# Performance work log

Measured on AMD Instinct MI355X. Metric: run time of the kernel, lower is better.

Reference implementation:

```python
import jax, jax.numpy as jnp
import numpy as np

N_NODES = 20000
N_EDGES = 320000
N_QUERY = 100000
D = 256


def _sage_conv(x, adj_row, adj_col, Wl, bl, Wr):
    # PyG SAGEConv with mean aggregation over SparseTensor adj_t:
    #   out = lin_l(mean_{j in N(i)} x_j) + lin_r(x_i)
    # adj_row = destination node, adj_col = source node.
    n = x.shape[0]
    msg = x[adj_col]                                        # [E, D] gather
    agg = jax.ops.segment_sum(msg, adj_row, num_segments=n)  # [N, D]
    deg = jax.ops.segment_sum(jnp.ones((adj_row.shape[0],), x.dtype), adj_row,
                              num_segments=n)
    agg = agg / jnp.maximum(deg, 1.0)[:, None]               # mean reduce
    return agg @ Wl + bl + x @ Wr


def setup_inputs() -> dict:
    key = jax.random.key(0)
    ks = jax.random.split(key, 12)
    s = 1.0 / np.sqrt(D)
    return {
        "adj_row": jax.random.randint(ks[0], (N_EDGES,), 0, N_NODES, dtype=jnp.int32),
        "adj_col": jax.random.randint(ks[1], (N_EDGES,), 0, N_NODES, dtype=jnp.int32),
        "edges": jax.random.randint(ks[2], (2, N_QUERY), 0, N_NODES, dtype=jnp.int32),
        "emb": jax.random.normal(ks[3], (N_NODES, D), jnp.float32),
        "W1l": jax.random.normal(ks[4], (D, D), jnp.float32) * s,
        "b1": jnp.zeros((D,), jnp.float32),
        "W1r": jax.random.normal(ks[5], (D, D), jnp.float32) * s,
        "W2l": jax.random.normal(ks[6], (D, D), jnp.float32) * s,
        "b2": jnp.zeros((D,), jnp.float32),
        "W2r": jax.random.normal(ks[7], (D, D), jnp.float32) * s,
        "Wp1": jax.random.normal(ks[8], (D, D), jnp.float32) * s,
        "bp1": jnp.zeros((D,), jnp.float32),
        "Wp2": jax.random.normal(ks[9], (D, 1), jnp.float32) * s,
        "bp2": jnp.zeros((1,), jnp.float32),
    }


def reference(adj_row, adj_col, edges, emb, W1l, b1, W1r, W2l, b2, W2r,
              Wp1, bp1, Wp2, bp2):
    # SAGE backbone (eval mode: dropout is identity)
    x = _sage_conv(emb, adj_row, adj_col, W1l, b1, W1r)
    x = jax.nn.relu(x)
    x = _sage_conv(x, adj_row, adj_col, W2l, b2, W2r)     # [N, D]
    # LinkPredictor: h = x_i * x_j -> MLP -> sigmoid
    h = x[edges[0]] * x[edges[1]]                          # [Q, D]
    h = jax.nn.relu(h @ Wp1 + bp1)
    return jax.nn.sigmoid(h @ Wp2 + bp2)                   # [Q, 1]
```

## Files before the change

### kernel.cpp

```cpp
#include <hip/hip_runtime.h>
#include <cstddef>

constexpr int NN = 20000;
constexpr int NE = 320000;
constexpr int NQ = 100000;
constexpr int DD = 256;
constexpr int NB = (NN + 255) / 256;
constexpr int CASTB = (NN * DD / 8 + 255) / 256;

typedef __attribute__((ext_vector_type(8))) short bf16x8;
typedef __attribute__((ext_vector_type(4))) float f32x4;
typedef __attribute__((ext_vector_type(4))) unsigned short u16x4;
typedef __attribute__((ext_vector_type(8))) unsigned short u16x8;

__device__ inline unsigned short f2bf(float f) {
    union { float f; unsigned u; } v; v.f = f;
    unsigned r = v.u + 0x7fffu + ((v.u >> 16) & 1u);
    return (unsigned short)(r >> 16);
}
__device__ inline float bf2f(unsigned short h) {
    union { unsigned u; float f; } t; t.u = ((unsigned)h) << 16;
    return t.f;
}

__global__ __launch_bounds__(256) void k_castpack(
    const float* __restrict__ x, unsigned short* __restrict__ y,
    int* __restrict__ deg,
    const float* __restrict__ w0, const float* __restrict__ w1,
    const float* __restrict__ w2, const float* __restrict__ w3,
    const float* __restrict__ w4,
    unsigned short* __restrict__ h0, unsigned short* __restrict__ h1,
    unsigned short* __restrict__ h2, unsigned short* __restrict__ h3,
    unsigned short* __restrict__ h4,
    unsigned short* __restrict__ l0, unsigned short* __restrict__ l1,
    unsigned short* __restrict__ l2, unsigned short* __restrict__ l3) {
    const int bid = blockIdx.x;
    if (bid < CASTB) {
        int i = bid * 256 + threadIdx.x;
        if (i < NN) deg[i] = 0;
        if (i >= NN * DD / 8) return;
        float4 f0 = *reinterpret_cast<const float4*>(x + (size_t)i * 8);
        float4 f1 = *reinterpret_cast<const float4*>(x + (size_t)i * 8 + 4);
        u16x8 o;
        o[0] = f2bf(f0.x); o[1] = f2bf(f0.y); o[2] = f2bf(f0.z); o[3] = f2bf(f0.w);
        o[4] = f2bf(f1.x); o[5] = f2bf(f1.y); o[6] = f2bf(f1.z); o[7] = f2bf(f1.w);
        *reinterpret_cast<u16x8*>(y + (size_t)i * 8) = o;
        return;
    }
    int mb = bid - CASTB;
    int m = mb >> 5;
    int idx = (mb & 31) * 256 + threadIdx.x;
    const float* W = (m == 0) ? w0 : (m == 1) ? w1 : (m == 2) ? w2 : (m == 3) ? w3 : w4;
    unsigned short* H = (m == 0) ? h0 : (m == 1) ? h1 : (m == 2) ? h2 : (m == 3) ? h3 : h4;
    unsigned short* L = (m == 0) ? l0 : (m == 1) ? l1 : (m == 2) ? l2 : (m == 3) ? l3 : nullptr;
    int t = idx >> 6, lane = idx & 63;
    int kt = t >> 4, nt = t & 15;
    int k0 = kt * 32 + (lane >> 4) * 8;
    int n = nt * 16 + (lane & 15);
    unsigned uh[4], ul[4];
#pragma unroll
    for (int i = 0; i < 4; ++i) {
        float fa = W[(size_t)(k0 + 2 * i) * DD + n];
        float fb = W[(size_t)(k0 + 2 * i + 1) * DD + n];
        unsigned short ha = f2bf(fa), hb = f2bf(fb);
        unsigned short la = f2bf(fa - bf2f(ha)), lb = f2bf(fb - bf2f(hb));
        uh[i] = (unsigned)ha | ((unsigned)hb << 16);
        ul[i] = (unsigned)la | ((unsigned)lb << 16);
    }
    *reinterpret_cast<uint4*>(H + (size_t)idx * 8) = make_uint4(uh[0], uh[1], uh[2], uh[3]);
    if (L)
        *reinterpret_cast<uint4*>(L + (size_t)idx * 8) = make_uint4(ul[0], ul[1], ul[2], ul[3]);
}

__global__ __launch_bounds__(256) void k_deg(const int* __restrict__ row,
                                             int* __restrict__ deg) {
    int e = blockIdx.x * 256 + threadIdx.x;
    if (e < NE) atomicAdd(&deg[row[e]], 1);
}

__global__ __launch_bounds__(256) void k_scan1(const int* __restrict__ deg,
                                               int* __restrict__ offs,
                                               int* __restrict__ bsum) {
    __shared__ int wsum[4];
    const int tid = threadIdx.x, lane = tid & 63, wid = tid >> 6;
    int i = blockIdx.x * 256 + tid;
    int v = (i < NN) ? deg[i] : 0;
    int sc = v;
#pragma unroll
    for (int d = 1; d < 64; d <<= 1) {
        int t = __shfl_up(sc, d);
        if (lane >= d) sc += t;
    }
    if (lane == 63) wsum[wid] = sc;
    __syncthreads();
    int wpre = 0;
    for (int w = 0; w < wid; ++w) wpre += wsum[w];
    if (i < NN) offs[i] = wpre + sc - v;
    if (tid == 255) bsum[blockIdx.x] = wpre + sc;
}

__global__ __launch_bounds__(256) void k_scan2(int* __restrict__ bsum) {
    __shared__ int wsum[4];
    const int tid = threadIdx.x, lane = tid & 63, wid = tid >> 6;
    int v = (tid < NB) ? bsum[tid] : 0;
    int sc = v;
#pragma unroll
    for (int d = 1; d < 64; d <<= 1) {
        int t = __shfl_up(sc, d);
        if (lane >= d) sc += t;
    }
    if (lane == 63) wsum[wid] = sc;
    __syncthreads();
    int wpre = 0;
    for (int w = 0; w < wid; ++w) wpre += wsum[w];
    if (tid < NB) bsum[tid] = wpre + sc - v;
}

__global__ __launch_bounds__(256) void k_scan3(const int* __restrict__ deg,
                                               const int* __restrict__ bsum,
                                               int* __restrict__ offs,
                                               int* __restrict__ cursor,
                                               float* __restrict__ recip) {
    int i = blockIdx.x * 256 + threadIdx.x;
    if (i < NN) {
        int o = offs[i] + bsum[i >> 8];
        offs[i] = o;
        cursor[i] = o;
        recip[i] = 1.0f / fmaxf((float)deg[i], 1.0f);
    }
    if (i == 0) offs[NN] = NE;
}

__global__ __launch_bounds__(256) void k_fill(const int* __restrict__ row,
                                              const int* __restrict__ col,
                                              int* __restrict__ cursor,
                                              int* __restrict__ scol) {
    int e = blockIdx.x * 256 + threadIdx.x;
    if (e < NE) {
        int r = row[e];
        int p = atomicAdd(&cursor[r], 1);
        scol[p] = col[e];
    }
}

__global__ __launch_bounds__(256) void k_lin(
    const unsigned short* __restrict__ A,
    const unsigned short* __restrict__ Wlh, const unsigned short* __restrict__ Wll,
    const unsigned short* __restrict__ Wrh, const unsigned short* __restrict__ Wrl,
    unsigned short* __restrict__ P, unsigned short* __restrict__ Q) {
    const int ns   = blockIdx.x & 7;
    const int mblk = blockIdx.x >> 3;
    const int wave = threadIdx.x >> 6;
    const int lane = threadIdx.x & 63;
    const int row0 = mblk * 128 + wave * 32;
    const int kcol = (lane >> 4) * 8;
    const int ar0 = min(row0 + (lane & 15), NN - 1);
    const int ar1 = min(row0 + 16 + (lane & 15), NN - 1);

    f32x4 accP[2][2], accQ[2][2];
#pragma unroll
    for (int mt = 0; mt < 2; ++mt)
#pragma unroll
        for (int nt = 0; nt < 2; ++nt) {
            accP[mt][nt] = {0, 0, 0, 0};
            accQ[mt][nt] = {0, 0, 0, 0};
        }

#pragma unroll 2
    for (int kt = 0; kt < 8; ++kt) {
        bf16x8 a0 = *reinterpret_cast<const bf16x8*>(A + (size_t)ar0 * DD + kt * 32 + kcol);
        bf16x8 a1 = *reinterpret_cast<const bf16x8*>(A + (size_t)ar1 * DD + kt * 32 + kcol);
#pragma unroll
        for (int nt = 0; nt < 2; ++nt) {
            const size_t fo = ((size_t)((kt * 16 + ns * 2 + nt) * 64 + lane)) * 8;
            bf16x8 blh = *reinterpret_cast<const bf16x8*>(Wlh + fo);
            bf16x8 bll = *reinterpret_cast<const bf16x8*>(Wll + fo);
            bf16x8 brh = *reinterpret_cast<const bf16x8*>(Wrh + fo);
            bf16x8 brl = *reinterpret_cast<const bf16x8*>(Wrl + fo);
            accP[0][nt] = __builtin_amdgcn_mfma_f32_16x16x32_bf16(a0, blh, accP[0][nt], 0, 0, 0);
            accP[1][nt] = __builtin_amdgcn_mfma_f32_16x16x32_bf16(a1, blh, accP[1][nt], 0, 0, 0);
            accP[0][nt] = __builtin_amdgcn_mfma_f32_16x16x32_bf16(a0, bll, accP[0][nt], 0, 0, 0);
            accP[1][nt] = __builtin_amdgcn_mfma_f32_16x16x32_bf16(a1, bll, accP[1][nt], 0, 0, 0);
            accQ[0][nt] = __builtin_amdgcn_mfma_f32_16x16x32_bf16(a0, brh, accQ[0][nt], 0, 0, 0);
            accQ[1][nt] = __builtin_amdgcn_mfma_f32_16x16x32_bf16(a1, brh, accQ[1][nt], 0, 0, 0);
            accQ[0][nt] = __builtin_amdgcn_mfma_f32_16x16x32_bf16(a0, brl, accQ[0][nt], 0, 0, 0);
            accQ[1][nt] = __builtin_amdgcn_mfma_f32_16x16x32_bf16(a1, brl, accQ[1][nt], 0, 0, 0);
        }
    }

    const int n0 = lane & 15;
    const int rg = (lane >> 4) * 4;
#pragma unroll
    for (int mt = 0; mt < 2; ++mt)
#pragma unroll
        for (int nt = 0; nt < 2; ++nt) {
            int n = (ns * 2 + nt) * 16 + n0;
#pragma unroll
            for (int j = 0; j < 4; ++j) {
                int r = row0 + mt * 16 + rg + j;
                if (r < NN) {
                    P[(size_t)r * DD + n] = f2bf(accP[mt][nt][j]);
                    Q[(size_t)r * DD + n] = f2bf(accQ[mt][nt][j]);
                }
            }
        }
}

template <int RELU>
__global__ __launch_bounds__(256) void k_gath(const int* __restrict__ offs,
                                              const int* __restrict__ scol,
                                              const float* __restrict__ recip,
                                              const unsigned short* __restrict__ P,
                                              const unsigned short* __restrict__ Q,
                                              const float* __restrict__ b,
                                              unsigned short* __restrict__ out) {
    int node = blockIdx.x * 4 + (threadIdx.x >> 6);
    int lane = threadIdx.x & 63;
    if (node >= NN) return;
    int s = offs[node];
    int e = offs[node + 1];
    const int half = lane >> 5;
    const int l32 = lane & 31;
    float a0[8] = {0,0,0,0,0,0,0,0}, a1[8] = {0,0,0,0,0,0,0,0};
    float a2[8] = {0,0,0,0,0,0,0,0}, a3[8] = {0,0,0,0,0,0,0,0};
    int p = s;
    for (; p + 7 < e; p += 8) {
        int base = p + 4 * half;
        int c0 = scol[base], c1 = scol[base + 1], c2 = scol[base + 2], c3 = scol[base + 3];
        u16x8 v0 = *reinterpret_cast<const u16x8*>(P + (size_t)c0 * DD + l32 * 8);
        u16x8 v1 = *reinterpret_cast<const u16x8*>(P + (size_t)c1 * DD + l32 * 8);
        u16x8 v2 = *reinterpret_cast<const u16x8*>(P + (size_t)c2 * DD + l32 * 8);
        u16x8 v3 = *reinterpret_cast<const u16x8*>(P + (size_t)c3 * DD + l32 * 8);
#pragma unroll
        for (int i = 0; i < 8; ++i) {
            a0[i] += bf2f(v0[i]); a1[i] += bf2f(v1[i]);
            a2[i] += bf2f(v2[i]); a3[i] += bf2f(v3[i]);
        }
    }
    for (; p + 1 < e; p += 2) {
        int c0 = scol[p + half];
        u16x8 v0 = *reinterpret_cast<const u16x8*>(P + (size_t)c0 * DD + l32 * 8);
#pragma unroll
        for (int i = 0; i < 8; ++i) a0[i] += bf2f(v0[i]);
    }
    if (p < e && half == 0) {
        int c0 = scol[p];
        u16x8 v0 = *reinterpret_cast<const u16x8*>(P + (size_t)c0 * DD + l32 * 8);
#pragma unroll
        for (int i = 0; i < 8; ++i) a1[i] += bf2f(v0[i]);
    }
    float rc = recip[node];
    u16x8 q = *reinterpret_cast<const u16x8*>(Q + (size_t)node * DD + l32 * 8);
    float4 b0 = *reinterpret_cast<const float4*>(b + l32 * 8);
    float4 b1 = *reinterpret_cast<const float4*>(b + l32 * 8 + 4);
    float bb[8] = {b0.x, b0.y, b0.z, b0.w, b1.x, b1.y, b1.z, b1.w};
    u16x8 o;
#pragma unroll
    for (int i = 0; i < 8; ++i) {
        float t = a0[i] + a1[i] + a2[i] + a3[i];
        t += __shfl_xor(t, 32);
        t = t * rc + bf2f(q[i]) + bb[i];
        if (RELU) t = fmaxf(t, 0.0f);
        o[i] = f2bf(t);
    }
    if (half == 0)
        *reinterpret_cast<u16x8*>(out + (size_t)node * DD + l32 * 8) = o;
}

__global__ __launch_bounds__(512, 4) void k_pred(const int* __restrict__ edges,
                                                 const unsigned short* __restrict__ x2,
                                                 const unsigned short* __restrict__ Wp1p,
                                                 const float* __restrict__ bp1,
                                                 const float* __restrict__ Wp2,
                                                 const float* __restrict__ bp2,
                                                 float* __restrict__ out) {
    __shared__ unsigned short sh[128 * 256];
    const int tid = threadIdx.x;
    const int wave = tid >> 6;
    const int lane = tid & 63;
    const int q0 = blockIdx.x * 128;

    const int grow = tid >> 4;
    const int t16 = tid & 15;
#pragma unroll
    for (int s = 0; s < 4; ++s) {
        int r = s * 32 + grow;
        int q = q0 + r;
        u16x8 p0 = {0, 0, 0, 0, 0, 0, 0, 0};
        u16x8 p1 = {0, 0, 0, 0, 0, 0, 0, 0};
        if (q < NQ) {
            int a = edges[q];
            int c = edges[NQ + q];
            const unsigned short* pa = x2 + (size_t)a * DD + t16 * 16;
            const unsigned short* pc = x2 + (size_t)c * DD + t16 * 16;
            u16x8 ua0 = *reinterpret_cast<const u16x8*>(pa);
            u16x8 ua1 = *reinterpret_cast<const u16x8*>(pa + 8);
            u16x8 uc0 = *reinterpret_cast<const u16x8*>(pc);
            u16x8 uc1 = *reinterpret_cast<const u16x8*>(pc + 8);
#pragma unroll
            for (int i = 0; i < 8; ++i) {
                p0[i] = f2bf(bf2f(ua0[i]) * bf2f(uc0[i]));
                p1[i] = f2bf(bf2f(ua1[i]) * bf2f(uc1[i]));
            }
        }
        int swz = (r & 7) << 3;
        *reinterpret_cast<u16x8*>(&sh[r * 256 + ((t16 * 16) ^ swz)]) = p0;
        *reinterpret_cast<u16x8*>(&sh[r * 256 + ((t16 * 16 + 8) ^ swz)]) = p1;
    }
    __syncthreads();

    f32x4 acc[8][2];
#pragma unroll
    for (int m = 0; m < 8; ++m)
#pragma unroll
        for (int n = 0; n < 2; ++n) acc[m][n] = {0, 0, 0, 0};

    const int akoff = (lane >> 4) * 8;
    const int arl = lane & 15;
    for (int kt = 0; kt < 8; ++kt) {
        bf16x8 af[8];
#pragma unroll
        for (int m = 0; m < 8; ++m) {
            int row = m * 16 + arl;
            af[m] = *reinterpret_cast<const bf16x8*>(
                &sh[row * 256 + ((kt * 32 + akoff) ^ ((row & 7) << 3))]);
        }
#pragma unroll
        for (int ntl = 0; ntl < 2; ++ntl) {
            int nt = wave * 2 + ntl;
            bf16x8 bfrag = *reinterpret_cast<const bf16x8*>(
                Wp1p + ((size_t)((kt * 16 + nt) * 64 + lane)) * 8);
#pragma unroll
            for (int m = 0; m < 8; ++m)
                acc[m][ntl] = __builtin_amdgcn_mfma_f32_16x16x32_bf16(af[m], bfrag, acc[m][ntl], 0, 0, 0);
        }
    }

    float rs[8][4];
#pragma unroll
    for (int m = 0; m < 8; ++m)
#pragma unroll
        for (int j = 0; j < 4; ++j) rs[m][j] = 0.0f;
#pragma unroll
    for (int ntl = 0; ntl < 2; ++ntl) {
        int n = (wave * 2 + ntl) * 16 + (lane & 15);
        float bias = bp1[n];
        float w2 = Wp2[n];
#pragma unroll
        for (int m = 0; m < 8; ++m)
#pragma unroll
            for (int j = 0; j < 4; ++j)
                rs[m][j] += fmaxf(acc[m][ntl][j] + bias, 0.0f) * w2;
    }
#pragma unroll
    for (int msk = 1; msk < 16; msk <<= 1) {
#pragma unroll
        for (int m = 0; m < 8; ++m)
#pragma unroll
            for (int j = 0; j < 4; ++j) rs[m][j] += __shfl_xor(rs[m][j], msk);
    }

    float* psum = reinterpret_cast<float*>(sh);
    __syncthreads();
    if ((lane & 15) == 0) {
        int rg = (lane >> 4) * 4;
#pragma unroll
        for (int m = 0; m < 8; ++m)
#pragma unroll
            for (int j = 0; j < 4; ++j)
                psum[wave * 128 + m * 16 + rg + j] = rs[m][j];
    }
    __syncthreads();

    if (tid < 128) {
        int q = q0 + tid;
        if (q < NQ) {
            float z = bp2[0];
#pragma unroll
            for (int w = 0; w < 8; ++w) z += psum[w * 128 + tid];
            out[q] = 1.0f / (1.0f + expf(-z));
        }
    }
}

extern "C" void kernel_launch(void* const* d_in, const int* in_sizes, int n_in,
                              void* d_out, int out_size, void* d_ws, size_t ws_size,
                              hipStream_t stream) {
    const int*   adj_row = (const int*)d_in[0];
    const int*   adj_col = (const int*)d_in[1];
    const int*   edges   = (const int*)d_in[2];
    const float* emb     = (const float*)d_in[3];
    const float* W1l     = (const float*)d_in[4];
    const float* b1      = (const float*)d_in[5];
    const float* W1r     = (const float*)d_in[6];
    const float* W2l     = (const float*)d_in[7];
    const float* b2      = (const float*)d_in[8];
    const float* W2r     = (const float*)d_in[9];
    const float* Wp1     = (const float*)d_in[10];
    const float* bp1     = (const float*)d_in[11];
    const float* Wp2     = (const float*)d_in[12];
    const float* bp2     = (const float*)d_in[13];
    float* out = (float*)d_out;

    const size_t featH = (size_t)NN * DD * 2;
    const size_t packBytes = (size_t)DD * DD * 2;

    char* ws = (char*)d_ws;
    size_t off = 0;
    unsigned short* P  = (unsigned short*)(ws + off); off += featH;
    unsigned short* Q  = (unsigned short*)(ws + off); off += featH;
    unsigned short* x1 = (unsigned short*)(ws + off); off += featH;
    unsigned short* xh = (unsigned short*)(ws + off); off += featH;
    int*   deg    = (int*)(ws + off);   off += (size_t)NN * 4;
    int*   offs   = (int*)(ws + off);   off += (size_t)(NN + 1) * 4;
    int*   cursor = (int*)(ws + off);   off += (size_t)NN * 4;
    float* recip  = (float*)(ws + off); off += (size_t)NN * 4;
    int*   bsum   = (int*)(ws + off);   off += (size_t)NB * 4;
    int*   scol   = (int*)(ws + off);   off += (size_t)NE * 4;
    unsigned short* Wp1p = (unsigned short*)(ws + off); off += packBytes;
    unsigned short* pk[8];
    for (int i = 0; i < 8; ++i) { pk[i] = (unsigned short*)(ws + off); off += packBytes; }

    const int MB8 = ((NN + 127) / 128) * 8;

    k_castpack<<<CASTB + 160, 256, 0, stream>>>(emb, xh, deg,
                                                W1l, W1r, W2l, W2r, Wp1,
                                                pk[0], pk[2], pk[4], pk[6], Wp1p,
                                                pk[1], pk[3], pk[5], pk[7]);
    k_deg<<<(NE + 255) / 256, 256, 0, stream>>>(adj_row, deg);
    k_scan1<<<NB, 256, 0, stream>>>(deg, offs, bsum);
    k_scan2<<<1, 256, 0, stream>>>(bsum);
    k_scan3<<<NB, 256, 0, stream>>>(deg, bsum, offs, cursor, recip);
    k_fill<<<(NE + 255) / 256, 256, 0, stream>>>(adj_row, adj_col, cursor, scol);

    k_lin<<<MB8, 256, 0, stream>>>(xh, pk[0], pk[1], pk[2], pk[3], P, Q);
    k_gath<1><<<(NN + 3) / 4, 256, 0, stream>>>(offs, scol, recip, P, Q, b1, x1);

    unsigned short* x2 = xh;
    k_lin<<<MB8, 256, 0, stream>>>(x1, pk[4], pk[5], pk[6], pk[7], P, Q);
    k_gath<0><<<(NN + 3) / 4, 256, 0, stream>>>(offs, scol, recip, P, Q, b2, x2);

    k_pred<<<(NQ + 127) / 128, 512, 0, stream>>>(edges, x2, Wp1p, bp1, Wp2, bp2, out);
}
```

Before: 198.0 us.

## Fuse three-pass scan into one decoupled-lookback kernel, retile predictor MFMA, add setprio

Replaces the three scan kernels with one kernel that publishes each block's total through a flag array and spins on the flags of earlier blocks, removing two launches. The predictor GEMM changes from each wave owning all 8 row tiles and 2 column tiles to a 2x4 wave grid owning 4x4 tiles, which changes fragment reuse and the partial-sum reduction. s_setprio is raised around the MFMA block in k_lin. The spin-wait assumes all earlier blocks make progress, which holds only because the grid is small (79 blocks).

```diff
diff --git a/kernel.cpp b/kernel.cpp
--- a/kernel.cpp
+++ b/kernel.cpp
@@ -25,7 +25,7 @@
 
 __global__ __launch_bounds__(256) void k_castpack(
     const float* __restrict__ x, unsigned short* __restrict__ y,
-    int* __restrict__ deg,
+    int* __restrict__ deg, int* __restrict__ bflag,
     const float* __restrict__ w0, const float* __restrict__ w1,
     const float* __restrict__ w2, const float* __restrict__ w3,
     const float* __restrict__ w4,
@@ -38,6 +38,7 @@
     if (bid < CASTB) {
         int i = bid * 256 + threadIdx.x;
         if (i < NN) deg[i] = 0;
+        if (bid == 0 && threadIdx.x < NB) bflag[threadIdx.x] = 0;
         if (i >= NN * DD / 8) return;
         float4 f0 = *reinterpret_cast<const float4*>(x + (size_t)i * 8);
         float4 f1 = *reinterpret_cast<const float4*>(x + (size_t)i * 8 + 4);
@@ -78,12 +79,16 @@
     if (e < NE) atomicAdd(&deg[row[e]], 1);
 }
 
-__global__ __launch_bounds__(256) void k_scan1(const int* __restrict__ deg,
+__global__ __launch_bounds__(256) void k_scanf(const int* __restrict__ deg,
                                                int* __restrict__ offs,
-                                               int* __restrict__ bsum) {
+                                               int* __restrict__ cursor,
+                                               float* __restrict__ recip,
+                                               int* __restrict__ bflag) {
     __shared__ int wsum[4];
+    __shared__ int s_pre;
     const int tid = threadIdx.x, lane = tid & 63, wid = tid >> 6;
-    int i = blockIdx.x * 256 + tid;
+    const int bid = blockIdx.x;
+    int i = bid * 256 + tid;
     int v = (i < NN) ? deg[i] : 0;
     int sc = v;
 #pragma unroll
@@ -95,38 +100,31 @@
     __syncthreads();
     int wpre = 0;
     for (int w = 0; w < wid; ++w) wpre += wsum[w];
-    if (i < NN) offs[i] = wpre + sc - v;
-    if (tid == 255) bsum[blockIdx.x] = wpre + sc;
-}
-
-__global__ __launch_bounds__(256) void k_scan2(int* __restrict__ bsum) {
-    __shared__ int wsum[4];
-    const int tid = threadIdx.x, lane = tid & 63, wid = tid >> 6;
-    int v = (tid < NB) ? bsum[tid] : 0;
-    int sc = v;
-#pragma unroll
-    for (int d = 1; d < 64; d <<= 1) {
-        int t = __shfl_up(sc, d);
-        if (lane >= d) sc += t;
-    }
-    if (lane == 63) wsum[wid] = sc;
-    __syncthreads();
-    int wpre = 0;
-    for (int w = 0; w < wid; ++w) wpre += wsum[w];
-    if (tid < NB) bsum[tid] = wpre + sc - v;
-}
-
-__global__ __launch_bounds__(256) void k_scan3(const int* __restrict__ deg,
-                                               const int* __restrict__ bsum,
-                                               int* __restrict__ offs,
-                                               int* __restrict__ cursor,
-                                               float* __restrict__ recip) {
-    int i = blockIdx.x * 256 + threadIdx.x;
+    int btot = wsum[0] + wsum[1] + wsum[2] + wsum[3];
+
+    if (tid == 0) atomicExch(&bflag[bid], btot + 1);
+
+    int myv = 0;
+    if (tid < bid) {
+        int f;
+        do { f = atomicAdd(&bflag[tid], 0); } while (f == 0);
+        myv = f - 1;
+    }
+    int rs = myv;
+#pragma unroll
+    for (int d = 1; d < 64; d <<= 1) rs += __shfl_xor(rs, d);
+    __syncthreads();
+    if (lane == 0) wsum[wid] = rs;
+    __syncthreads();
+    if (tid == 0) s_pre = wsum[0] + wsum[1] + wsum[2] + wsum[3];
+    __syncthreads();
+    int pre = s_pre;
+
     if (i < NN) {
-        int o = offs[i] + bsum[i >> 8];
+        int o = pre + wpre + sc - v;
         offs[i] = o;
         cursor[i] = o;
-        recip[i] = 1.0f / fmaxf((float)deg[i], 1.0f);
+        recip[i] = 1.0f / fmaxf((float)v, 1.0f);
     }
     if (i == 0) offs[NN] = NE;
 }
@@ -177,6 +175,7 @@
             bf16x8 bll = *reinterpret_cast<const bf16x8*>(Wll + fo);
             bf16x8 brh = *reinterpret_cast<const bf16x8*>(Wrh + fo);
             bf16x8 brl = *reinterpret_cast<const bf16x8*>(Wrl + fo);
+            __builtin_amdgcn_s_setprio(1);
             accP[0][nt] = __builtin_amdgcn_mfma_f32_16x16x32_bf16(a0, blh, accP[0][nt], 0, 0, 0);
             accP[1][nt] = __builtin_amdgcn_mfma_f32_16x16x32_bf16(a1, blh, accP[1][nt], 0, 0, 0);
             accP[0][nt] = __builtin_amdgcn_mfma_f32_16x16x32_bf16(a0, bll, accP[0][nt], 0, 0, 0);
@@ -185,6 +184,7 @@
             accQ[1][nt] = __builtin_amdgcn_mfma_f32_16x16x32_bf16(a1, brh, accQ[1][nt], 0, 0, 0);
             accQ[0][nt] = __builtin_amdgcn_mfma_f32_16x16x32_bf16(a0, brl, accQ[0][nt], 0, 0, 0);
             accQ[1][nt] = __builtin_amdgcn_mfma_f32_16x16x32_bf16(a1, brl, accQ[1][nt], 0, 0, 0);
+            __builtin_amdgcn_s_setprio(0);
         }
     }
 
@@ -309,53 +309,55 @@
     }
     __syncthreads();
 
-    f32x4 acc[8][2];
-#pragma unroll
-    for (int m = 0; m < 8; ++m)
-#pragma unroll
-        for (int n = 0; n < 2; ++n) acc[m][n] = {0, 0, 0, 0};
+    const int mg = wave >> 2;
+    const int ng = wave & 3;
+    f32x4 acc[4][4];
+#pragma unroll
+    for (int m = 0; m < 4; ++m)
+#pragma unroll
+        for (int n = 0; n < 4; ++n) acc[m][n] = {0, 0, 0, 0};
 
     const int akoff = (lane >> 4) * 8;
     const int arl = lane & 15;
     for (int kt = 0; kt < 8; ++kt) {
-        bf16x8 af[8];
-#pragma unroll
-        for (int m = 0; m < 8; ++m) {
-            int row = m * 16 + arl;
+        bf16x8 af[4];
+#pragma unroll
+        for (int m = 0; m < 4; ++m) {
+            int row = (mg * 4 + m) * 16 + arl;
             af[m] = *reinterpret_cast<const bf16x8*>(
                 &sh[row * 256 + ((kt * 32 + akoff) ^ ((row & 7) << 3))]);
         }
 #pragma unroll
-        for (int ntl = 0; ntl < 2; ++ntl) {
-            int nt = wave * 2 + ntl;
+        for (int n = 0; n < 4; ++n) {
+            int nt = ng * 4 + n;
             bf16x8 bfrag = *reinterpret_cast<const bf16x8*>(
                 Wp1p + ((size_t)((kt * 16 + nt) * 64 + lane)) * 8);
 #pragma unroll
-            for (int m = 0; m < 8; ++m)
-                acc[m][ntl] = __builtin_amdgcn_mfma_f32_16x16x32_bf16(af[m], bfrag, acc[m][ntl], 0, 0, 0);
-        }
-    }
-
-    float rs[8][4];
-#pragma unroll
-    for (int m = 0; m < 8; ++m)
+            for (int m = 0; m < 4; ++m)
+                acc[m][n] = __builtin_amdgcn_mfma_f32_16x16x32_bf16(af[m], bfrag, acc[m][n], 0, 0, 0);
+        }
+    }
+
+    float rs[4][4];
+#pragma unroll
+    for (int m = 0; m < 4; ++m)
 #pragma unroll
         for (int j = 0; j < 4; ++j) rs[m][j] = 0.0f;
 #pragma unroll
-    for (int ntl = 0; ntl < 2; ++ntl) {
-        int n = (wave * 2 + ntl) * 16 + (lane & 15);
-        float bias = bp1[n];
-        float w2 = Wp2[n];
-#pragma unroll
-        for (int m = 0; m < 8; ++m)
+    for (int n = 0; n < 4; ++n) {
+        int nc = (ng * 4 + n) * 16 + (lane & 15);
+        float bias = bp1[nc];
+        float w2 = Wp2[nc];
+#pragma unroll
+        for (int m = 0; m < 4; ++m)
 #pragma unroll
             for (int j = 0; j < 4; ++j)
-                rs[m][j] += fmaxf(acc[m][ntl][j] + bias, 0.0f) * w2;
+                rs[m][j] += fmaxf(acc[m][n][j] + bias, 0.0f) * w2;
     }
 #pragma unroll
     for (int msk = 1; msk < 16; msk <<= 1) {
 #pragma unroll
-        for (int m = 0; m < 8; ++m)
+        for (int m = 0; m < 4; ++m)
 #pragma unroll
             for (int j = 0; j < 4; ++j) rs[m][j] += __shfl_xor(rs[m][j], msk);
     }
@@ -365,10 +367,10 @@
     if ((lane & 15) == 0) {
         int rg = (lane >> 4) * 4;
 #pragma unroll
-        for (int m = 0; m < 8; ++m)
+        for (int m = 0; m < 4; ++m)
 #pragma unroll
             for (int j = 0; j < 4; ++j)
-                psum[wave * 128 + m * 16 + rg + j] = rs[m][j];
+                psum[ng * 128 + (mg * 4 + m) * 16 + rg + j] = rs[m][j];
     }
     __syncthreads();
 
@@ -377,7 +379,7 @@
         if (q < NQ) {
             float z = bp2[0];
 #pragma unroll
-            for (int w = 0; w < 8; ++w) z += psum[w * 128 + tid];
+            for (int w = 0; w < 4; ++w) z += psum[w * 128 + tid];
             out[q] = 1.0f / (1.0f + expf(-z));
         }
     }
@@ -415,7 +417,7 @@
     int*   offs   = (int*)(ws + off);   off += (size_t)(NN + 1) * 4;
     int*   cursor = (int*)(ws + off);   off += (size_t)NN * 4;
     float* recip  = (float*)(ws + off); off += (size_t)NN * 4;
-    int*   bsum   = (int*)(ws + off);   off += (size_t)NB * 4;
+    int*   bflag  = (int*)(ws + off);   off += (size_t)NB * 4;
     int*   scol   = (int*)(ws + off);   off += (size_t)NE * 4;
     unsigned short* Wp1p = (unsigned short*)(ws + off); off += packBytes;
     unsigned short* pk[8];
@@ -423,14 +425,12 @@
 
     const int MB8 = ((NN + 127) / 128) * 8;
 
-    k_castpack<<<CASTB + 160, 256, 0, stream>>>(emb, xh, deg,
+    k_castpack<<<CASTB + 160, 256, 0, stream>>>(emb, xh, deg, bflag,
                                                 W1l, W1r, W2l, W2r, Wp1,
                                                 pk[0], pk[2], pk[4], pk[6], Wp1p,
                                                 pk[1], pk[3], pk[5], pk[7]);
     k_deg<<<(NE + 255) / 256, 256, 0, stream>>>(adj_row, deg);
-    k_scan1<<<NB, 256, 0, stream>>>(deg, offs, bsum);
-    k_scan2<<<1, 256, 0, stream>>>(bsum);
-    k_scan3<<<NB, 256, 0, stream>>>(deg, bsum, offs, cursor, recip);
+    k_scanf<<<NB, 256, 0, stream>>>(deg, offs, cursor, recip, bflag);
     k_fill<<<(NE + 255) / 256, 256, 0, stream>>>(adj_row, adj_col, cursor, scol);
 
     k_lin<<<MB8, 256, 0, stream>>>(xh, pk[0], pk[1], pk[2], pk[3], P, Q);
```

Measured after the change: 188.8 us. 4.6% less time.
